# Kernel tuning notes

Measured on AMD Instinct MI355X. Metric: run time of the kernel, lower is better.

Reference implementation:

```python
import jax, jax.numpy as jnp
import numpy as np

N = 50000          # nodes
E = 800000         # edges (avg degree 16)
ROLE_DIM = 16
LAY_DIM = 16
G_IN = 96          # graph_in
H = 96             # hidden_channels (two layers of 96)
G_OUT = 96         # graph_out
HID = 256          # dense hidden_dim
NUM_ROLES = 120
MAX_LAYOUT = 1025


def _lin_params(k, out_d, in_d, bias=True):
    kw, kb = jax.random.split(k)
    s = 1.0 / np.sqrt(in_d)
    W = jax.random.uniform(kw, (out_d, in_d), jnp.float32, -s, s)
    if bias:
        b = jax.random.uniform(kb, (out_d,), jnp.float32, -s, s)
        return W, b
    return W


def setup_inputs() -> dict:
    key = jax.random.key(0)
    ks = jax.random.split(key, 16)
    x_layout = jax.random.randint(ks[0], (N, 4), 0, MAX_LAYOUT)
    x_role = jax.random.randint(ks[1], (N,), 0, NUM_ROLES)
    edge_index = jax.random.randint(ks[2], (2, E), 0, N)
    layout_emb = jax.random.normal(ks[3], (MAX_LAYOUT, LAY_DIM), jnp.float32)
    role_emb = jax.random.normal(ks[4], (NUM_ROLES, ROLE_DIM), jnp.float32)
    lin_W, lin_b = _lin_params(ks[5], G_IN, ROLE_DIM + 4 * LAY_DIM)
    c0_lW, c0_lb = _lin_params(ks[6], H, G_IN)
    c0_rW = _lin_params(ks[7], H, G_IN, bias=False)
    c1_lW, c1_lb = _lin_params(ks[8], H, H)
    c1_rW = _lin_params(ks[9], H, H, bias=False)
    c2_lW, c2_lb = _lin_params(ks[10], G_OUT, H)
    c2_rW = _lin_params(ks[11], G_OUT, H, bias=False)
    d0_W, d0_b = _lin_params(ks[12], HID, G_OUT)
    d1_W, d1_b = _lin_params(ks[13], HID, HID)
    d2_W, d2_b = _lin_params(ks[14], 1, HID)
    return dict(x_layout=x_layout, x_role=x_role, edge_index=edge_index,
                layout_emb=layout_emb, role_emb=role_emb,
                lin_W=lin_W, lin_b=lin_b,
                c0_lW=c0_lW, c0_lb=c0_lb, c0_rW=c0_rW,
                c1_lW=c1_lW, c1_lb=c1_lb, c1_rW=c1_rW,
                c2_lW=c2_lW, c2_lb=c2_lb, c2_rW=c2_rW,
                d0_W=d0_W, d0_b=d0_b, d1_W=d1_W, d1_b=d1_b,
                d2_W=d2_W, d2_b=d2_b)


def _sage(x, src, dst, lW, lb, rW):
    # SAGEConv (mean aggr): out = lin_l(mean_{j->i} x_j) + lin_r(x_i)
    msg = x[src]                                               # [E, D] gather
    ssum = jax.ops.segment_sum(msg, dst, num_segments=N)       # [N, D]
    cnt = jax.ops.segment_sum(jnp.ones((src.shape[0],), x.dtype), dst,
                              num_segments=N)                  # [N]
    agg = ssum / jnp.maximum(cnt, 1.0)[:, None]
    return agg @ lW.T + lb + x @ rW.T


def reference(x_layout, x_role, edge_index, layout_emb, role_emb,
              lin_W, lin_b,
              c0_lW, c0_lb, c0_rW,
              c1_lW, c1_lb, c1_rW,
              c2_lW, c2_lb, c2_rW,
              d0_W, d0_b, d1_W, d1_b, d2_W, d2_b):
    # embed + concat: [N, 4*16] layout embeds + [N, 16] role embed
    lay = layout_emb[x_layout].reshape(x_layout.shape[0], 4 * LAY_DIM)
    x = jnp.concatenate([lay, role_emb[x_role]], axis=1)       # [N, 80]
    x = x @ lin_W.T + lin_b                                    # [N, G_IN]
    # masked_select with x_role != -100: all indices valid here -> identity
    src, dst = edge_index[0], edge_index[1]
    x = jax.nn.relu(_sage(x, src, dst, c0_lW, c0_lb, c0_rW))
    x = jax.nn.relu(_sage(x, src, dst, c1_lW, c1_lb, c1_rW))
    x = jax.nn.relu(_sage(x, src, dst, c2_lW, c2_lb, c2_rW))
    # dense head (dropout p=0 -> identity)
    x = jax.nn.relu(x @ d0_W.T + d0_b)
    x = jax.nn.relu(x @ d1_W.T + d1_b)
    return x @ d2_W.T + d2_b                                   # [N, 1]
```

## Files before the change

kernel.cpp:

```cpp
#include <hip/hip_runtime.h>
#include <cstddef>


#define NB 256

using f16x4 = __attribute__((ext_vector_type(4))) _Float16;
using f32x4 = __attribute__((ext_vector_type(4))) float;

__global__ __launch_bounds__(NB) void count_int_kernel(const int* __restrict__ dst,
                                                       int* __restrict__ cnt, int E) {
    int e = blockIdx.x * NB + threadIdx.x;
    if (e < E) atomicAdd(&cnt[dst[e]], 1);
}

__global__ __launch_bounds__(NB) void scan_part1(const int* __restrict__ cnt,
                                                 int* __restrict__ part, int n) {
    __shared__ int ws[4];
    const int tid = threadIdx.x;
    const int base = blockIdx.x * 2048 + tid * 8;
    int s = 0;
#pragma unroll
    for (int q = 0; q < 8; ++q) {
        int i = base + q;
        if (i < n) s += cnt[i];
    }
#pragma unroll
    for (int off = 1; off < 64; off <<= 1) s += __shfl_xor(s, off);
    if ((tid & 63) == 0) ws[tid >> 6] = s;
    __syncthreads();
    if (tid == 0) part[blockIdx.x] = ws[0] + ws[1] + ws[2] + ws[3];
}

__global__ __launch_bounds__(64) void scan_part2(int* __restrict__ part,
                                                 int* __restrict__ rowptr,
                                                 int nb, int n) {
    const int lane = threadIdx.x;
    int v = (lane < nb) ? part[lane] : 0;
    int incl = v;
#pragma unroll
    for (int off = 1; off < 64; off <<= 1) {
        int u = __shfl_up(incl, off);
        if (lane >= off) incl += u;
    }
    if (lane < nb) part[lane] = incl - v;
    if (lane == 63) rowptr[n] = incl;
}

__global__ __launch_bounds__(NB) void scan_part3(const int* __restrict__ cnt,
                                                 const int* __restrict__ part,
                                                 int* __restrict__ rowptr,
                                                 int* __restrict__ cursor, int n) {
    __shared__ int ws[4];
    const int tid = threadIdx.x;
    const int lane = tid & 63, w = tid >> 6;
    const int base = blockIdx.x * 2048 + tid * 8;
    int loc[8];
    int s = 0;
#pragma unroll
    for (int q = 0; q < 8; ++q) {
        int i = base + q;
        int v = (i < n) ? cnt[i] : 0;
        loc[q] = s;
        s += v;
    }
    int incl = s;
#pragma unroll
    for (int off = 1; off < 64; off <<= 1) {
        int u = __shfl_up(incl, off);
        if (lane >= off) incl += u;
    }
    if (lane == 63) ws[w] = incl;
    __syncthreads();
    int woff = 0;
    for (int i = 0; i < w; ++i) woff += ws[i];
    int gbase = part[blockIdx.x] + woff + (incl - s);
#pragma unroll
    for (int q = 0; q < 8; ++q) {
        int i = base + q;
        if (i < n) {
            int v = gbase + loc[q];
            rowptr[i] = v;
            cursor[i] = v;
        }
    }
}

__global__ __launch_bounds__(NB) void fill_csr_kernel(const int* __restrict__ src,
                                                      const int* __restrict__ dst,
                                                      int* __restrict__ cursor,
                                                      int* __restrict__ col, int E) {
    int e = blockIdx.x * NB + threadIdx.x;
    if (e >= E) return;
    int p = atomicAdd(&cursor[dst[e]], 1);
    col[p] = src[e];
}

__global__ __launch_bounds__(NB) void gather_mean_kernel(
    const float* __restrict__ X, const int* __restrict__ rowptr,
    const int* __restrict__ col, float* __restrict__ G, int N) {
    int idx = blockIdx.x * NB + threadIdx.x;
    int node = idx / 24;
    if (node >= N) return;
    int c = idx - node * 24;
    const int s = rowptr[node], pe = rowptr[node + 1];
    float4 acc = {0.f, 0.f, 0.f, 0.f};
    int p = s;
    for (; p + 3 < pe; p += 4) {
        int j0 = col[p], j1 = col[p + 1], j2 = col[p + 2], j3 = col[p + 3];
        float4 v0 = *reinterpret_cast<const float4*>(&X[(size_t)j0 * 96 + 4 * c]);
        float4 v1 = *reinterpret_cast<const float4*>(&X[(size_t)j1 * 96 + 4 * c]);
        float4 v2 = *reinterpret_cast<const float4*>(&X[(size_t)j2 * 96 + 4 * c]);
        float4 v3 = *reinterpret_cast<const float4*>(&X[(size_t)j3 * 96 + 4 * c]);
        acc.x += (v0.x + v1.x) + (v2.x + v3.x);
        acc.y += (v0.y + v1.y) + (v2.y + v3.y);
        acc.z += (v0.z + v1.z) + (v2.z + v3.z);
        acc.w += (v0.w + v1.w) + (v2.w + v3.w);
    }
    for (; p < pe; ++p) {
        int j = col[p];
        float4 v = *reinterpret_cast<const float4*>(&X[(size_t)j * 96 + 4 * c]);
        acc.x += v.x; acc.y += v.y; acc.z += v.z; acc.w += v.w;
    }
    int deg = pe - s;
    float inv = (deg > 0) ? 1.f / (float)deg : 0.f;
    acc.x *= inv; acc.y *= inv; acc.z *= inv; acc.w *= inv;
    *reinterpret_cast<float4*>(&G[(size_t)node * 96 + 4 * c]) = acc;
}

__device__ inline void cvt_split(float4 f, f16x4& hi, f16x4& lo) {
    _Float16 h0 = (_Float16)f.x, h1 = (_Float16)f.y;
    _Float16 h2 = (_Float16)f.z, h3 = (_Float16)f.w;
    hi = (f16x4){h0, h1, h2, h3};
    lo = (f16x4){(_Float16)(f.x - (float)h0), (_Float16)(f.y - (float)h1),
                 (_Float16)(f.z - (float)h2), (_Float16)(f.w - (float)h3)};
}

template <int K, int OUT, int TC, int BK, bool RELU, bool SAGE, bool EMB, bool FDOT>
__global__ __launch_bounds__(NB) void gemm_mfma(
    const float* __restrict__ X, const float* __restrict__ G,
    const float* __restrict__ Wx, const float* __restrict__ Wg,
    const float* __restrict__ bias,
    const int* __restrict__ xl, const int* __restrict__ xr,
    const float* __restrict__ lemb, const float* __restrict__ remb,
    const float* __restrict__ d2w, const float* __restrict__ d2b,
    float* __restrict__ Y, int nrows) {
    constexpr int BM = 64;
    constexpr int BN = 2 * TC * 16;
    constexpr int CT = OUT / BN;
    constexpr int KT = SAGE ? 2 * K : K;
    constexpr int QX = BK / 4;
    constexpr int ST = BK + 4;
    __shared__ alignas(16) _Float16 Xhi[BM][ST];
    __shared__ alignas(16) _Float16 Xlo[BM][ST];
    __shared__ alignas(16) _Float16 Whi[BN][ST];
    __shared__ alignas(16) _Float16 Wlo[BN][ST];

    const int t = threadIdx.x;
    const int lane = t & 63;
    const int wave = t >> 6;
    const int lm = lane & 15, lg = lane >> 4;
    const int wm = (wave >> 1) * 32;
    const int wn = (wave & 1) * (TC * 16);

    const int bid = blockIdx.x;
    const int rowBase = (bid / CT) * BM;
    const int colTile = bid % CT;
    const int colBase = colTile * BN;

    f32x4 acc[2][TC];
#pragma unroll
    for (int tr = 0; tr < 2; ++tr)
#pragma unroll
        for (int tc = 0; tc < TC; ++tc) acc[tr][tc] = (f32x4){0.f, 0.f, 0.f, 0.f};

    for (int k0 = 0; k0 < KT; k0 += BK) {
        const bool isG = SAGE && (k0 >= K);
        const float* __restrict__ Xp = isG ? G : X;
        const float* __restrict__ Wp = isG ? Wg : Wx;
        const int kl = isG ? (k0 - K) : k0;

        for (int v = t; v < BM * QX; v += NB) {
            int q = v % QX, m = v / QX;
            int r = rowBase + m;
            float4 f = {0.f, 0.f, 0.f, 0.f};
            if (r < nrows) {
                if (EMB) {
                    int kk = kl + 4 * q;
                    if (kk < 64) {
                        int l = kk >> 4, c = kk & 15;
                        f = *reinterpret_cast<const float4*>(
                            &lemb[(size_t)xl[r * 4 + l] * 16 + c]);
                    } else {
                        f = *reinterpret_cast<const float4*>(
                            &remb[(size_t)xr[r] * 16 + (kk - 64)]);
                    }
                } else {
                    f = *reinterpret_cast<const float4*>(&Xp[(size_t)r * K + kl + 4 * q]);
                }
            }
            f16x4 hi, lo;
            cvt_split(f, hi, lo);
            *reinterpret_cast<f16x4*>(&Xhi[m][4 * q]) = hi;
            *reinterpret_cast<f16x4*>(&Xlo[m][4 * q]) = lo;
        }
        for (int v = t; v < BN * QX; v += NB) {
            int q = v % QX, n = v / QX;
            float4 f = *reinterpret_cast<const float4*>(
                &Wp[(size_t)(colBase + n) * K + kl + 4 * q]);
            f16x4 hi, lo;
            cvt_split(f, hi, lo);
            *reinterpret_cast<f16x4*>(&Whi[n][4 * q]) = hi;
            *reinterpret_cast<f16x4*>(&Wlo[n][4 * q]) = lo;
        }
        __syncthreads();

#pragma unroll
        for (int g = 0; g < BK / 16; ++g) {
            f16x4 ah[2], al[2], bh[TC], bl[TC];
#pragma unroll
            for (int tr = 0; tr < 2; ++tr) {
                ah[tr] = *reinterpret_cast<const f16x4*>(
                    &Xhi[wm + tr * 16 + lm][g * 16 + 4 * lg]);
                al[tr] = *reinterpret_cast<const f16x4*>(
                    &Xlo[wm + tr * 16 + lm][g * 16 + 4 * lg]);
            }
#pragma unroll
            for (int tc = 0; tc < TC; ++tc) {
                bh[tc] = *reinterpret_cast<const f16x4*>(
                    &Whi[wn + tc * 16 + lm][g * 16 + 4 * lg]);
                bl[tc] = *reinterpret_cast<const f16x4*>(
                    &Wlo[wn + tc * 16 + lm][g * 16 + 4 * lg]);
            }
#pragma unroll
            for (int tr = 0; tr < 2; ++tr)
#pragma unroll
                for (int tc = 0; tc < TC; ++tc) {
                    acc[tr][tc] = __builtin_amdgcn_mfma_f32_16x16x16f16(
                        ah[tr], bh[tc], acc[tr][tc], 0, 0, 0);
                    acc[tr][tc] = __builtin_amdgcn_mfma_f32_16x16x16f16(
                        ah[tr], bl[tc], acc[tr][tc], 0, 0, 0);
                    acc[tr][tc] = __builtin_amdgcn_mfma_f32_16x16x16f16(
                        al[tr], bh[tc], acc[tr][tc], 0, 0, 0);
                }
        }
        __syncthreads();
    }

    if (!FDOT) {
#pragma unroll
        for (int tr = 0; tr < 2; ++tr)
#pragma unroll
            for (int tc = 0; tc < TC; ++tc) {
                int c = colBase + wn + tc * 16 + lm;
#pragma unroll
                for (int j = 0; j < 4; ++j) {
                    int r = rowBase + wm + tr * 16 + 4 * lg + j;
                    if (r >= nrows) continue;
                    float v = acc[tr][tc][j] + bias[c];
                    if (RELU) v = fmaxf(v, 0.f);
                    Y[(size_t)r * OUT + c] = v;
                }
            }
    } else {
#pragma unroll
        for (int tr = 0; tr < 2; ++tr) {
            float p[4] = {0.f, 0.f, 0.f, 0.f};
#pragma unroll
            for (int tc = 0; tc < TC; ++tc) {
                int c = colBase + wn + tc * 16 + lm;
                float bv = bias[c];
                float dw = d2w[c];
#pragma unroll
                for (int j = 0; j < 4; ++j) {
                    float v = fmaxf(acc[tr][tc][j] + bv, 0.f);
                    p[j] += v * dw;
                }
            }
#pragma unroll
            for (int j = 0; j < 4; ++j) {
                float s = p[j];
#pragma unroll
                for (int off = 1; off < 16; off <<= 1) s += __shfl_xor(s, off);
                int r = rowBase + wm + tr * 16 + 4 * lg + j;
                if (lm == 0 && r < nrows) {
                    float extra = (colTile == 0 && wn == 0) ? d2b[0] : 0.f;
                    atomicAdd(&Y[r], s + extra);
                }
            }
        }
    }
}

extern "C" void kernel_launch(void* const* d_in, const int* in_sizes, int n_in,
                              void* d_out, int out_size, void* d_ws, size_t ws_size,
                              hipStream_t stream) {
    const int*   x_layout = (const int*)d_in[0];
    const int*   x_role   = (const int*)d_in[1];
    const int*   ei       = (const int*)d_in[2];
    const float* lemb     = (const float*)d_in[3];
    const float* remb     = (const float*)d_in[4];
    const float* lin_W    = (const float*)d_in[5];
    const float* lin_b    = (const float*)d_in[6];
    const float* c0_lW    = (const float*)d_in[7];
    const float* c0_lb    = (const float*)d_in[8];
    const float* c0_rW    = (const float*)d_in[9];
    const float* c1_lW    = (const float*)d_in[10];
    const float* c1_lb    = (const float*)d_in[11];
    const float* c1_rW    = (const float*)d_in[12];
    const float* c2_lW    = (const float*)d_in[13];
    const float* c2_lb    = (const float*)d_in[14];
    const float* c2_rW    = (const float*)d_in[15];
    const float* d0_W     = (const float*)d_in[16];
    const float* d0_b     = (const float*)d_in[17];
    const float* d1_W     = (const float*)d_in[18];
    const float* d1_b     = (const float*)d_in[19];
    const float* d2_W     = (const float*)d_in[20];
    const float* d2_b     = (const float*)d_in[21];

    const int N = in_sizes[1];
    const int E = in_sizes[2] / 2;
    const int* src = ei;
    const int* dst = ei + E;

    float* ws     = (float*)d_ws;
    float* H0     = ws;
    int*   rowptr = (int*)d_ws;
    int*   cursor = rowptr + (N + 1);
    int*   col    = cursor + N;
    int*   part   = col + E;
    float* A      = ws + (size_t)256 * N;
    float* B      = A + (size_t)96 * N;
    float* C      = B + (size_t)96 * N;

    const dim3 blk(NB);
    const int rt64 = (N + 63) / 64;
    const int nbScan = (N + 2047) / 2048;
    const dim3 gE((E + NB - 1) / NB);
    const dim3 gGather(((size_t)N * 24 + NB - 1) / NB);

    hipMemsetAsync(cursor, 0, (size_t)N * sizeof(int), stream);
    count_int_kernel<<<gE, blk, 0, stream>>>(dst, cursor, E);
    scan_part1<<<dim3(nbScan), blk, 0, stream>>>(cursor, part, N);
    scan_part2<<<dim3(1), dim3(64), 0, stream>>>(part, rowptr, nbScan, N);
    scan_part3<<<dim3(nbScan), blk, 0, stream>>>(cursor, part, rowptr, cursor, N);
    fill_csr_kernel<<<gE, blk, 0, stream>>>(src, dst, cursor, col, E);

    gemm_mfma<80, 96, 3, 16, false, false, true, false>
        <<<dim3(rt64), blk, 0, stream>>>(
        nullptr, nullptr, lin_W, nullptr, lin_b,
        x_layout, x_role, lemb, remb, nullptr, nullptr, A, N);

    gather_mean_kernel<<<gGather, blk, 0, stream>>>(A, rowptr, col, B, N);
    gemm_mfma<96, 96, 3, 32, true, true, false, false>
        <<<dim3(rt64), blk, 0, stream>>>(
        A, B, c0_rW, c0_lW, c0_lb, nullptr, nullptr, nullptr, nullptr,
        nullptr, nullptr, C, N);

    gather_mean_kernel<<<gGather, blk, 0, stream>>>(C, rowptr, col, B, N);
    gemm_mfma<96, 96, 3, 32, true, true, false, false>
        <<<dim3(rt64), blk, 0, stream>>>(
        C, B, c1_rW, c1_lW, c1_lb, nullptr, nullptr, nullptr, nullptr,
        nullptr, nullptr, A, N);

    gather_mean_kernel<<<gGather, blk, 0, stream>>>(A, rowptr, col, B, N);
    gemm_mfma<96, 96, 3, 32, true, true, false, false>
        <<<dim3(rt64), blk, 0, stream>>>(
        A, B, c2_rW, c2_lW, c2_lb, nullptr, nullptr, nullptr, nullptr,
        nullptr, nullptr, C, N);

    gemm_mfma<96, 256, 4, 32, true, false, false, false>
        <<<dim3(rt64 * 2), blk, 0, stream>>>(
        C, nullptr, d0_W, nullptr, d0_b, nullptr, nullptr, nullptr, nullptr,
        nullptr, nullptr, H0, N);

    hipMemsetAsync(d_out, 0, (size_t)N * sizeof(float), stream);
    gemm_mfma<256, 256, 4, 32, true, false, false, true>
        <<<dim3(rt64 * 2), blk, 0, stream>>>(
        H0, nullptr, d1_W, nullptr, d1_b, nullptr, nullptr, nullptr, nullptr,
        d2_W, d2_b, (float*)d_out, N);
}
```

Baseline: 499.5 us.

## Prefetch next K-tile into registers while computing current tile in GEMM

Restructures the GEMM main loop into a software pipeline: global loads for the next K-step go into registers (xreg/wreg) before the MFMA compute of the current step, and the fp16 hi/lo split plus shared-memory store happens at the top of the next iteration. This is meant to hide global and gather load latency behind the MFMA work. The cost is higher register pressure, which may lower occupancy.

```diff
diff --git a/kernel.cpp b/kernel.cpp
--- a/kernel.cpp
+++ b/kernel.cpp
@@ -150,6 +150,8 @@
     constexpr int KT = SAGE ? 2 * K : K;
     constexpr int QX = BK / 4;
     constexpr int ST = BK + 4;
+    constexpr int RX = (BM * QX + NB - 1) / NB;
+    constexpr int RW = (BN * QX + NB - 1) / NB;
     __shared__ alignas(16) _Float16 Xhi[BM][ST];
     __shared__ alignas(16) _Float16 Xlo[BM][ST];
     __shared__ alignas(16) _Float16 Whi[BN][ST];
@@ -167,52 +169,87 @@
     const int colTile = bid % CT;
     const int colBase = colTile * BN;
 
-    f32x4 acc[2][TC];
-#pragma unroll
-    for (int tr = 0; tr < 2; ++tr)
-#pragma unroll
-        for (int tc = 0; tc < TC; ++tc) acc[tr][tc] = (f32x4){0.f, 0.f, 0.f, 0.f};
-
-    for (int k0 = 0; k0 < KT; k0 += BK) {
+    float4 xreg[RX], wreg[RW];
+
+    auto loadstep = [&](int k0) {
         const bool isG = SAGE && (k0 >= K);
         const float* __restrict__ Xp = isG ? G : X;
         const float* __restrict__ Wp = isG ? Wg : Wx;
         const int kl = isG ? (k0 - K) : k0;
-
-        for (int v = t; v < BM * QX; v += NB) {
-            int q = v % QX, m = v / QX;
-            int r = rowBase + m;
-            float4 f = {0.f, 0.f, 0.f, 0.f};
-            if (r < nrows) {
-                if (EMB) {
-                    int kk = kl + 4 * q;
-                    if (kk < 64) {
-                        int l = kk >> 4, c = kk & 15;
-                        f = *reinterpret_cast<const float4*>(
-                            &lemb[(size_t)xl[r * 4 + l] * 16 + c]);
+#pragma unroll
+        for (int rr = 0; rr < RX; ++rr) {
+            int v = t + rr * NB;
+            if (v < BM * QX) {
+                int q = v % QX, m = v / QX;
+                int r = rowBase + m;
+                float4 f = {0.f, 0.f, 0.f, 0.f};
+                if (r < nrows) {
+                    if (EMB) {
+                        int kk = kl + 4 * q;
+                        if (kk < 64) {
+                            int l = kk >> 4, c = kk & 15;
+                            f = *reinterpret_cast<const float4*>(
+                                &lemb[(size_t)xl[r * 4 + l] * 16 + c]);
+                        } else {
+                            f = *reinterpret_cast<const float4*>(
+                                &remb[(size_t)xr[r] * 16 + (kk - 64)]);
+                        }
                     } else {
                         f = *reinterpret_cast<const float4*>(
-                            &remb[(size_t)xr[r] * 16 + (kk - 64)]);
+                            &Xp[(size_t)r * K + kl + 4 * q]);
                     }
-                } else {
-                    f = *reinterpret_cast<const float4*>(&Xp[(size_t)r * K + kl + 4 * q]);
                 }
-            }
-            f16x4 hi, lo;
-            cvt_split(f, hi, lo);
-            *reinterpret_cast<f16x4*>(&Xhi[m][4 * q]) = hi;
-            *reinterpret_cast<f16x4*>(&Xlo[m][4 * q]) = lo;
-        }
-        for (int v = t; v < BN * QX; v += NB) {
-            int q = v % QX, n = v / QX;
-            float4 f = *reinterpret_cast<const float4*>(
-                &Wp[(size_t)(colBase + n) * K + kl + 4 * q]);
-            f16x4 hi, lo;
-            cvt_split(f, hi, lo);
-            *reinterpret_cast<f16x4*>(&Whi[n][4 * q]) = hi;
-            *reinterpret_cast<f16x4*>(&Wlo[n][4 * q]) = lo;
-        }
+                xreg[rr] = f;
+            }
+        }
+#pragma unroll
+        for (int rr = 0; rr < RW; ++rr) {
+            int v = t + rr * NB;
+            if (v < BN * QX) {
+                int q = v % QX, n = v / QX;
+                wreg[rr] = *reinterpret_cast<const float4*>(
+                    &Wp[(size_t)(colBase + n) * K + kl + 4 * q]);
+            }
+        }
+    };
+
+    auto storestep = [&]() {
+#pragma unroll
+        for (int rr = 0; rr < RX; ++rr) {
+            int v = t + rr * NB;
+            if (v < BM * QX) {
+                int q = v % QX, m = v / QX;
+                f16x4 hi, lo;
+                cvt_split(xreg[rr], hi, lo);
+                *reinterpret_cast<f16x4*>(&Xhi[m][4 * q]) = hi;
+                *reinterpret_cast<f16x4*>(&Xlo[m][4 * q]) = lo;
+            }
+        }
+#pragma unroll
+        for (int rr = 0; rr < RW; ++rr) {
+            int v = t + rr * NB;
+            if (v < BN * QX) {
+                int q = v % QX, n = v / QX;
+                f16x4 hi, lo;
+                cvt_split(wreg[rr], hi, lo);
+                *reinterpret_cast<f16x4*>(&Whi[n][4 * q]) = hi;
+                *reinterpret_cast<f16x4*>(&Wlo[n][4 * q]) = lo;
+            }
+        }
+    };
+
+    f32x4 acc[2][TC];
+#pragma unroll
+    for (int tr = 0; tr < 2; ++tr)
+#pragma unroll
+        for (int tc = 0; tc < TC; ++tc) acc[tr][tc] = (f32x4){0.f, 0.f, 0.f, 0.f};
+
+    loadstep(0);
+    for (int k0 = 0; k0 < KT; k0 += BK) {
+        if (k0 > 0) __syncthreads();
+        storestep();
         __syncthreads();
+        if (k0 + BK < KT) loadstep(k0 + BK);
 
 #pragma unroll
         for (int g = 0; g < BK / 16; ++g) {
@@ -243,7 +280,6 @@
                         al[tr], bh[tc], acc[tr][tc], 0, 0, 0);
                 }
         }
-        __syncthreads();
     }
 
     if (!FDOT) {
```

New measurement: 500.3 us. About the same (+0.2%).
